# Kernel tuning notes

Measured on AMD Instinct MI355X. Metric: run time of the kernel, lower is better.

## Reference

```python
import jax, jax.numpy as jnp
import numpy as np

N_NODES = 100000
N_EDGES = 3200000
OUT_CH = 128
X_DIM = 128


def setup_inputs() -> dict:
    key = jax.random.key(0)
    k1, k2, k3, k4 = jax.random.split(key, 4)
    x = jax.random.normal(k1, (N_NODES, X_DIM), dtype=jnp.float32)
    edge_index = jax.random.randint(k2, (2, N_EDGES), 0, N_NODES, dtype=jnp.int64)
    # torch nn.Linear(num_nodes, out_channels): weight [out, N], bias [out]
    W_weight = jax.random.normal(k3, (OUT_CH, N_NODES), dtype=jnp.float32) * (1.0 / np.sqrt(N_NODES))
    W_bias = jax.random.normal(k4, (OUT_CH,), dtype=jnp.float32) * 0.01
    return {"x": x, "edge_index": edge_index, "W_weight": W_weight, "W_bias": W_bias}


def reference(x, edge_index, W_weight, W_bias):
    """LINK forward: logits = A @ W.T + b, A = sparse COO adjacency from edge_index.

    A[r, c] = 1 for each edge (r, c), so row r of the output is
    sum_{c in neighbors(r)} W.T[c] + b  -> gather + segment_sum (SpMM).
    """
    N = x.shape[0]
    row, col = edge_index[0], edge_index[1]
    Wt = W_weight.T  # [N, out]
    gathered = Wt[col]  # [E, out] irregular gather
    logits = jax.ops.segment_sum(gathered, row, num_segments=N) + W_bias  # [N, out]
    return logits
```

## Files before the change

kernel.cpp:

```cpp
#include <hip/hip_runtime.h>


#define NCHUNK 256
#define STRIDE 13312
#define MAXB 1600
#define CAP 3072

__global__ __launch_bounds__(256) void absmax_kernel(const float* __restrict__ W,
                                                     int n4,
                                                     unsigned int* __restrict__ amax) {
    int i = blockIdx.x * blockDim.x + threadIdx.x;
    int stride = gridDim.x * blockDim.x;
    float m = 0.f;
    const float4* W4 = (const float4*)W;
    for (; i < n4; i += stride) {
        float4 v = W4[i];
        m = fmaxf(m, fmaxf(fmaxf(fabsf(v.x), fabsf(v.y)),
                           fmaxf(fabsf(v.z), fabsf(v.w))));
    }
    for (int off = 32; off > 0; off >>= 1) m = fmaxf(m, __shfl_xor(m, off));
    if ((threadIdx.x & 63) == 0) atomicMax(amax, __float_as_uint(m));
}

__global__ __launch_bounds__(256) void quant_kernel(const float* __restrict__ W,
                                                    unsigned char* __restrict__ Wt8,
                                                    const unsigned int* __restrict__ amax,
                                                    int N) {
    __shared__ float tile[128][33];
    int cx = threadIdx.x;
    int oy = threadIdx.y;
    int c = blockIdx.x * 32 + cx;
    for (int k = 0; k < 16; ++k) {
        int o = oy * 16 + k;
        tile[o][cx] = (c < N) ? W[(size_t)o * N + c] : 0.f;
    }
    __syncthreads();
    float M = __uint_as_float(*amax);
    float si = (M > 0.f) ? 127.f / M : 0.f;
    if (c < N) {
        unsigned int w[4];
#pragma unroll
        for (int d = 0; d < 4; ++d) {
            unsigned int acc = 0;
#pragma unroll
            for (int b = 0; b < 4; ++b) {
                int o = oy * 16 + d * 4 + b;
                int qi = __float2int_rn(tile[o][cx] * si) + 128;
                acc |= ((unsigned int)(qi & 0xff)) << (8 * b);
            }
            w[d] = acc;
        }
        *(uint4*)(Wt8 + (size_t)c * 128 + oy * 16) =
            make_uint4(w[0], w[1], w[2], w[3]);
    }
}

__global__ __launch_bounds__(1024) void sortchunk(const int* __restrict__ row,
                                                  const int* __restrict__ col,
                                                  int E, int chr_, int nbuck,
                                                  unsigned* __restrict__ packed,
                                                  unsigned* __restrict__ runinfo) {
    __shared__ unsigned g2[STRIDE];
    __shared__ int lh[MAXB];
    __shared__ int ls[MAXB];
    __shared__ int cur[MAXB];
    __shared__ int part[512];
    int c = blockIdx.x, tid = threadIdx.x;
    int s = c * chr_;
    int e = min(E, s + chr_);
    int cnt = e - s;
    for (int k = tid; k < nbuck; k += 1024) lh[k] = 0;
    __syncthreads();
    int rst[13], cst[13];
#pragma unroll
    for (int j = 0; j < 13; ++j) {
        int i = j * 1024 + tid;
        rst[j] = -1;
        cst[j] = 0;
        if (i < cnt) {
            rst[j] = row[s + i];
            cst[j] = col[s + i];
            atomicAdd(&lh[rst[j] >> 6], 1);
        }
    }
    __syncthreads();
    int v0 = 0, v1 = 0, v2 = 0, v3 = 0, mysum = 0;
    if (tid < 512) {
        int b4 = tid * 4;
        v0 = (b4 + 0 < nbuck) ? lh[b4 + 0] : 0;
        v1 = (b4 + 1 < nbuck) ? lh[b4 + 1] : 0;
        v2 = (b4 + 2 < nbuck) ? lh[b4 + 2] : 0;
        v3 = (b4 + 3 < nbuck) ? lh[b4 + 3] : 0;
        mysum = v0 + v1 + v2 + v3;
        part[tid] = mysum;
    }
    __syncthreads();
    for (int off = 1; off < 512; off <<= 1) {
        int t = 0;
        if (tid < 512 && tid >= off) t = part[tid - off];
        __syncthreads();
        if (tid < 512) part[tid] += t;
        __syncthreads();
    }
    if (tid < 512) {
        int excl = part[tid] - mysum;
        int b4 = tid * 4;
        if (b4 + 0 < nbuck) ls[b4 + 0] = excl;
        if (b4 + 1 < nbuck) ls[b4 + 1] = excl + v0;
        if (b4 + 2 < nbuck) ls[b4 + 2] = excl + v0 + v1;
        if (b4 + 3 < nbuck) ls[b4 + 3] = excl + v0 + v1 + v2;
    }
    __syncthreads();
    for (int k = tid; k < nbuck; k += 1024) cur[k] = ls[k];
    __syncthreads();
#pragma unroll
    for (int j = 0; j < 13; ++j) {
        if (rst[j] >= 0) {
            int p = atomicAdd(&cur[rst[j] >> 6], 1);
            g2[p] = ((unsigned)(rst[j] & 63) << 17) | (unsigned)cst[j];
        }
    }
    __syncthreads();
#pragma unroll
    for (int j = 0; j < 13; ++j) {
        int i = j * 1024 + tid;
        if (i < cnt) packed[(size_t)c * STRIDE + i] = g2[i];
    }
    for (int k = tid; k < nbuck; k += 1024)
        runinfo[(size_t)c * nbuck + k] =
            ((unsigned)ls[k] << 14) | (unsigned)lh[k];
}

__global__ __launch_bounds__(256) void spmm_fused(
    const unsigned* __restrict__ packed, const unsigned* __restrict__ runinfo,
    const unsigned char* __restrict__ Wt8, const float* __restrict__ bias,
    const unsigned int* __restrict__ amax, float* __restrict__ out, int N,
    int nbuck) {
    __shared__ unsigned stage[CAP];
    __shared__ unsigned g2[CAP];
    __shared__ int lensc[256];
    __shared__ int rhist[64];
    __shared__ int rs[65];
    __shared__ int cur[64];
    __shared__ int sc2[64];
    __shared__ int tot;
    int k = blockIdx.x, tid = threadIdx.x;
    unsigned ri = runinfo[(size_t)tid * nbuck + k];
    int len = ri & 0x3FFFu;
    int loc = ri >> 14;
    lensc[tid] = len;
    __syncthreads();
    for (int off = 1; off < 256; off <<= 1) {
        int t = (tid >= off) ? lensc[tid - off] : 0;
        __syncthreads();
        lensc[tid] += t;
        __syncthreads();
    }
    int dst = lensc[tid] - len;
    if (tid == 255) tot = lensc[255];
    __syncthreads();
    int cnt = min(tot, CAP);
    const unsigned* srcp = packed + (size_t)tid * STRIDE + loc;
    for (int j = 0; j < len; ++j)
        if (dst + j < CAP) stage[dst + j] = srcp[j];
    if (tid < 64) rhist[tid] = 0;
    __syncthreads();
    for (int i = tid; i < cnt; i += 256) atomicAdd(&rhist[stage[i] >> 17], 1);
    __syncthreads();
    if (tid < 64) sc2[tid] = rhist[tid];
    __syncthreads();
    for (int off = 1; off < 64; off <<= 1) {
        int t = 0;
        if (tid < 64 && tid >= off) t = sc2[tid - off];
        __syncthreads();
        if (tid < 64) sc2[tid] += t;
        __syncthreads();
    }
    if (tid < 64) {
        rs[tid] = sc2[tid] - rhist[tid];
        cur[tid] = rs[tid];
        if (tid == 63) rs[64] = sc2[63];
    }
    __syncthreads();
    for (int i = tid; i < cnt; i += 256) {
        unsigned v = stage[i];
        int p = atomicAdd(&cur[v >> 17], 1);
        g2[p] = (v & 0x1FFFFu) << 7;
    }
    __syncthreads();

    float sg = __uint_as_float(*amax) / 127.f;
    int wave = tid >> 6, lane = tid & 63;
    int h = lane >> 5;
    int lane4 = (lane & 31) * 4;

    for (int r = wave; r < 64; r += 4) {
        int gr = k * 64 + r;
        if (gr >= N) break;
        int js = rs[r], je = rs[r + 1];
        int m = je - js;
        int T = m >> 1;
        unsigned accA = 0, accB = 0;
        int idx = js + h;
        int t = 0;
        for (; t + 4 <= T; t += 4) {
            unsigned e0 = g2[idx + 0];
            unsigned e1 = g2[idx + 2];
            unsigned e2 = g2[idx + 4];
            unsigned e3 = g2[idx + 6];
            idx += 8;
            uint32_t u0 = *(const uint32_t*)(Wt8 + e0 + lane4);
            uint32_t u1 = *(const uint32_t*)(Wt8 + e1 + lane4);
            uint32_t u2 = *(const uint32_t*)(Wt8 + e2 + lane4);
            uint32_t u3 = *(const uint32_t*)(Wt8 + e3 + lane4);
            accA += (u0 & 0x00FF00FFu);
            accB += ((u0 >> 8) & 0x00FF00FFu);
            accA += (u1 & 0x00FF00FFu);
            accB += ((u1 >> 8) & 0x00FF00FFu);
            accA += (u2 & 0x00FF00FFu);
            accB += ((u2 >> 8) & 0x00FF00FFu);
            accA += (u3 & 0x00FF00FFu);
            accB += ((u3 >> 8) & 0x00FF00FFu);
        }
        for (; t < T; ++t) {
            unsigned e0 = g2[idx];
            idx += 2;
            uint32_t u0 = *(const uint32_t*)(Wt8 + e0 + lane4);
            accA += (u0 & 0x00FF00FFu);
            accB += ((u0 >> 8) & 0x00FF00FFu);
        }
        if ((m & 1) && h == 0) {
            unsigned e0 = g2[je - 1];
            uint32_t u0 = *(const uint32_t*)(Wt8 + e0 + lane4);
            accA += (u0 & 0x00FF00FFu);
            accB += ((u0 >> 8) & 0x00FF00FFu);
        }
        accA += __shfl_xor(accA, 32);
        accB += __shfl_xor(accB, 32);
        if (h == 0) {
            float fm = -128.f * (float)m;
            float4 b4 = *(const float4*)(bias + lane4);
            float4 res;
            res.x = fmaf(sg, (float)(accA & 0xffffu) + fm, b4.x);
            res.y = fmaf(sg, (float)(accB & 0xffffu) + fm, b4.y);
            res.z = fmaf(sg, (float)(accA >> 16) + fm, b4.z);
            res.w = fmaf(sg, (float)(accB >> 16) + fm, b4.w);
            *(float4*)(out + (size_t)gr * 128 + lane4) = res;
        }
    }
}

extern "C" void kernel_launch(void* const* d_in, const int* in_sizes, int n_in,
                              void* d_out, int out_size, void* d_ws,
                              size_t ws_size, hipStream_t stream) {
    const int* edge = (const int*)d_in[1];
    const float* W = (const float*)d_in[2];
    const float* bias = (const float*)d_in[3];
    float* out = (float*)d_out;

    const int N = in_sizes[0] / 128;
    const int E = in_sizes[1] / 2;
    const int* row = edge;
    const int* col = edge + E;

    const int nbuck = (N + 63) / 64;
    const int chr_ = (E + NCHUNK - 1) / NCHUNK;

    auto align16 = [](size_t v) { return (v + 15) & ~(size_t)15; };
    char* ws = (char*)d_ws;
    size_t off = 0;
    unsigned char* Wt8 = (unsigned char*)(ws + off);
    off = align16(off + (size_t)N * 128);
    unsigned* packed = (unsigned*)(ws + off);
    off = align16(off + (size_t)NCHUNK * STRIDE * sizeof(unsigned));
    unsigned* runinfo = (unsigned*)(ws + off);
    off = align16(off + (size_t)NCHUNK * nbuck * sizeof(unsigned));
    unsigned int* amax = (unsigned int*)(ws + off);
    off = align16(off + 16);

    hipMemsetAsync(amax, 0, sizeof(unsigned int), stream);

    absmax_kernel<<<1024, 256, 0, stream>>>(W, (128 * N) / 4, amax);
    {
        dim3 block(32, 8);
        dim3 grid((N + 31) / 32);
        quant_kernel<<<grid, block, 0, stream>>>(W, Wt8, amax, N);
    }
    sortchunk<<<NCHUNK, 1024, 0, stream>>>(row, col, E, chr_, nbuck, packed,
                                           runinfo);
    spmm_fused<<<nbuck, 256, 0, stream>>>(packed, runinfo, Wt8, bias, amax, out,
                                          N, nbuck);
}
```

Baseline: 193.4 us.

## Split edge bucketing into smaller chunks and add separate merge-runs kernel

Doubles the number of sort chunks and halves the block size, and drops the shared-memory staging buffer so edges are scattered straight to global memory by bucket offset. A new merge_runs kernel concatenates the per-chunk runs for each 64-row bucket into a contiguous colsorted buffer and records per-bucket counts. The SpMM kernel then reads that buffer instead of gathering 256 runs itself. The aim is more parallelism and occupancy in the sort, and simpler staging in the SpMM. The cost is an extra launch, an extra global round trip of the edge data, and uncoalesced scattered global writes in sortchunk.

```diff
diff --git a/kernel.cpp b/kernel.cpp
--- a/kernel.cpp
+++ b/kernel.cpp
@@ -1,8 +1,8 @@
 #include <hip/hip_runtime.h>
 
 
-#define NCHUNK 256
-#define STRIDE 13312
+#define NCHUNK 512
+#define STRIDE 6656
 #define MAXB 1600
 #define CAP 3072
 
@@ -55,26 +55,24 @@
     }
 }
 
-__global__ __launch_bounds__(1024) void sortchunk(const int* __restrict__ row,
-                                                  const int* __restrict__ col,
-                                                  int E, int chr_, int nbuck,
-                                                  unsigned* __restrict__ packed,
-                                                  unsigned* __restrict__ runinfo) {
-    __shared__ unsigned g2[STRIDE];
+__global__ __launch_bounds__(512) void sortchunk(const int* __restrict__ row,
+                                                 const int* __restrict__ col,
+                                                 int E, int chr_, int nbuck,
+                                                 unsigned* __restrict__ packed,
+                                                 unsigned* __restrict__ runinfo) {
     __shared__ int lh[MAXB];
     __shared__ int ls[MAXB];
-    __shared__ int cur[MAXB];
     __shared__ int part[512];
     int c = blockIdx.x, tid = threadIdx.x;
     int s = c * chr_;
     int e = min(E, s + chr_);
     int cnt = e - s;
-    for (int k = tid; k < nbuck; k += 1024) lh[k] = 0;
+    for (int k = tid; k < MAXB; k += 512) lh[k] = 0;
     __syncthreads();
     int rst[13], cst[13];
 #pragma unroll
     for (int j = 0; j < 13; ++j) {
-        int i = j * 1024 + tid;
+        int i = j * 512 + tid;
         rst[j] = -1;
         cst[j] = 0;
         if (i < cnt) {
@@ -84,88 +82,89 @@
         }
     }
     __syncthreads();
-    int v0 = 0, v1 = 0, v2 = 0, v3 = 0, mysum = 0;
-    if (tid < 512) {
-        int b4 = tid * 4;
-        v0 = (b4 + 0 < nbuck) ? lh[b4 + 0] : 0;
-        v1 = (b4 + 1 < nbuck) ? lh[b4 + 1] : 0;
-        v2 = (b4 + 2 < nbuck) ? lh[b4 + 2] : 0;
-        v3 = (b4 + 3 < nbuck) ? lh[b4 + 3] : 0;
-        mysum = v0 + v1 + v2 + v3;
-        part[tid] = mysum;
-    }
+    int b4 = tid * 4;
+    int v0 = (b4 + 0 < nbuck) ? lh[b4 + 0] : 0;
+    int v1 = (b4 + 1 < nbuck) ? lh[b4 + 1] : 0;
+    int v2 = (b4 + 2 < nbuck) ? lh[b4 + 2] : 0;
+    int v3 = (b4 + 3 < nbuck) ? lh[b4 + 3] : 0;
+    int mysum = v0 + v1 + v2 + v3;
+    part[tid] = mysum;
     __syncthreads();
     for (int off = 1; off < 512; off <<= 1) {
-        int t = 0;
-        if (tid < 512 && tid >= off) t = part[tid - off];
-        __syncthreads();
-        if (tid < 512) part[tid] += t;
-        __syncthreads();
-    }
-    if (tid < 512) {
+        int t = (tid >= off) ? part[tid - off] : 0;
+        __syncthreads();
+        part[tid] += t;
+        __syncthreads();
+    }
+    {
         int excl = part[tid] - mysum;
-        int b4 = tid * 4;
         if (b4 + 0 < nbuck) ls[b4 + 0] = excl;
         if (b4 + 1 < nbuck) ls[b4 + 1] = excl + v0;
         if (b4 + 2 < nbuck) ls[b4 + 2] = excl + v0 + v1;
         if (b4 + 3 < nbuck) ls[b4 + 3] = excl + v0 + v1 + v2;
     }
     __syncthreads();
-    for (int k = tid; k < nbuck; k += 1024) cur[k] = ls[k];
-    __syncthreads();
+    for (int k = tid; k < nbuck; k += 512)
+        runinfo[(size_t)c * nbuck + k] =
+            ((unsigned)ls[k] << 13) | (unsigned)lh[k];
+    __syncthreads();
+    unsigned* dst = packed + (size_t)c * STRIDE;
 #pragma unroll
     for (int j = 0; j < 13; ++j) {
         if (rst[j] >= 0) {
-            int p = atomicAdd(&cur[rst[j] >> 6], 1);
-            g2[p] = ((unsigned)(rst[j] & 63) << 17) | (unsigned)cst[j];
-        }
-    }
-    __syncthreads();
-#pragma unroll
-    for (int j = 0; j < 13; ++j) {
-        int i = j * 1024 + tid;
-        if (i < cnt) packed[(size_t)c * STRIDE + i] = g2[i];
-    }
-    for (int k = tid; k < nbuck; k += 1024)
-        runinfo[(size_t)c * nbuck + k] =
-            ((unsigned)ls[k] << 14) | (unsigned)lh[k];
+            int p = atomicAdd(&ls[rst[j] >> 6], 1);
+            dst[p] = ((unsigned)(rst[j] & 63) << 17) | (unsigned)cst[j];
+        }
+    }
+}
+
+__global__ __launch_bounds__(256) void merge_runs(const unsigned* __restrict__ packed,
+                                                  const unsigned* __restrict__ runinfo,
+                                                  int nbuck,
+                                                  unsigned* __restrict__ colsorted,
+                                                  int* __restrict__ cntk) {
+    __shared__ int part[256];
+    int k = blockIdx.x, tid = threadIdx.x;
+    unsigned ri0 = runinfo[(size_t)tid * nbuck + k];
+    unsigned ri1 = runinfo[(size_t)(tid + 256) * nbuck + k];
+    int len0 = ri0 & 0x1FFFu, loc0 = ri0 >> 13;
+    int len1 = ri1 & 0x1FFFu, loc1 = ri1 >> 13;
+    int mysum = len0 + len1;
+    part[tid] = mysum;
+    __syncthreads();
+    for (int off = 1; off < 256; off <<= 1) {
+        int t = (tid >= off) ? part[tid - off] : 0;
+        __syncthreads();
+        part[tid] += t;
+        __syncthreads();
+    }
+    int excl = part[tid] - mysum;
+    if (tid == 255) cntk[k] = min(part[255], CAP);
+    unsigned* dstp = colsorted + (size_t)k * CAP;
+    const unsigned* s0 = packed + (size_t)tid * STRIDE + loc0;
+    for (int j = 0; j < len0; ++j)
+        if (excl + j < CAP) dstp[excl + j] = s0[j];
+    int d1 = excl + len0;
+    const unsigned* s1 = packed + (size_t)(tid + 256) * STRIDE + loc1;
+    for (int j = 0; j < len1; ++j)
+        if (d1 + j < CAP) dstp[d1 + j] = s1[j];
 }
 
 __global__ __launch_bounds__(256) void spmm_fused(
-    const unsigned* __restrict__ packed, const unsigned* __restrict__ runinfo,
+    const unsigned* __restrict__ colsorted, const int* __restrict__ cntk,
     const unsigned char* __restrict__ Wt8, const float* __restrict__ bias,
-    const unsigned int* __restrict__ amax, float* __restrict__ out, int N,
-    int nbuck) {
-    __shared__ unsigned stage[CAP];
+    const unsigned int* __restrict__ amax, float* __restrict__ out, int N) {
     __shared__ unsigned g2[CAP];
-    __shared__ int lensc[256];
     __shared__ int rhist[64];
     __shared__ int rs[65];
     __shared__ int cur[64];
     __shared__ int sc2[64];
-    __shared__ int tot;
     int k = blockIdx.x, tid = threadIdx.x;
-    unsigned ri = runinfo[(size_t)tid * nbuck + k];
-    int len = ri & 0x3FFFu;
-    int loc = ri >> 14;
-    lensc[tid] = len;
-    __syncthreads();
-    for (int off = 1; off < 256; off <<= 1) {
-        int t = (tid >= off) ? lensc[tid - off] : 0;
-        __syncthreads();
-        lensc[tid] += t;
-        __syncthreads();
-    }
-    int dst = lensc[tid] - len;
-    if (tid == 255) tot = lensc[255];
-    __syncthreads();
-    int cnt = min(tot, CAP);
-    const unsigned* srcp = packed + (size_t)tid * STRIDE + loc;
-    for (int j = 0; j < len; ++j)
-        if (dst + j < CAP) stage[dst + j] = srcp[j];
+    int cnt = cntk[k];
+    const unsigned* src = colsorted + (size_t)k * CAP;
     if (tid < 64) rhist[tid] = 0;
     __syncthreads();
-    for (int i = tid; i < cnt; i += 256) atomicAdd(&rhist[stage[i] >> 17], 1);
+    for (int i = tid; i < cnt; i += 256) atomicAdd(&rhist[src[i] >> 17], 1);
     __syncthreads();
     if (tid < 64) sc2[tid] = rhist[tid];
     __syncthreads();
@@ -183,7 +182,7 @@
     }
     __syncthreads();
     for (int i = tid; i < cnt; i += 256) {
-        unsigned v = stage[i];
+        unsigned v = src[i];
         int p = atomicAdd(&cur[v >> 17], 1);
         g2[p] = (v & 0x1FFFFu) << 7;
     }
@@ -275,6 +274,10 @@
     off = align16(off + (size_t)NCHUNK * STRIDE * sizeof(unsigned));
     unsigned* runinfo = (unsigned*)(ws + off);
     off = align16(off + (size_t)NCHUNK * nbuck * sizeof(unsigned));
+    unsigned* colsorted = (unsigned*)(ws + off);
+    off = align16(off + (size_t)nbuck * CAP * sizeof(unsigned));
+    int* cntk = (int*)(ws + off);
+    off = align16(off + (size_t)nbuck * sizeof(int));
     unsigned int* amax = (unsigned int*)(ws + off);
     off = align16(off + 16);
 
@@ -286,8 +289,10 @@
         dim3 grid((N + 31) / 32);
         quant_kernel<<<grid, block, 0, stream>>>(W, Wt8, amax, N);
     }
-    sortchunk<<<NCHUNK, 1024, 0, stream>>>(row, col, E, chr_, nbuck, packed,
-                                           runinfo);
-    spmm_fused<<<nbuck, 256, 0, stream>>>(packed, runinfo, Wt8, bias, amax, out,
-                                          N, nbuck);
-}
+    sortchunk<<<NCHUNK, 512, 0, stream>>>(row, col, E, chr_, nbuck, packed,
+                                          runinfo);
+    merge_runs<<<nbuck, 256, 0, stream>>>(packed, runinfo, nbuck, colsorted,
+                                          cntk);
+    spmm_fused<<<nbuck, 256, 0, stream>>>(colsorted, cntk, Wt8, bias, amax, out,
+                                          N);
+}
```

Result: slower. 214.9 us (+11.2%).
